# Kernel tuning notes

Hardware: AMD Instinct MI355X
Metric: run time of the kernel (lower is better)

## Reference

```python
import jax, jax.numpy as jnp
import numpy as np

N_NODES = 100000   # number of graph nodes
N_EDGES = 1600000  # adjacency nnz (avg degree 16)
FEAT_NNZ = 1600000 # sparse feature nnz (~16 per node)
F_IN = 512
F_OUT = 128


def setup_inputs() -> dict:
    key = jax.random.key(0)
    k1, k2, k3, k4, k5, k6 = jax.random.split(key, 6)
    adj_indices = jax.random.randint(k1, (2, N_EDGES), 0, N_NODES, dtype=jnp.int64 if jax.config.jax_enable_x64 else jnp.int32)
    adj_values = jax.random.uniform(k2, (N_EDGES,), dtype=jnp.float32)
    feat_rows = jax.random.randint(k3, (FEAT_NNZ,), 0, N_NODES)
    feat_cols = jax.random.randint(k4, (FEAT_NNZ,), 0, F_IN)
    feat_values = jax.random.uniform(k5, (FEAT_NNZ,), dtype=jnp.float32)
    # xavier_uniform init of the dense weight, as in the torch module
    bound = float(np.sqrt(6.0 / (F_IN + F_OUT)))
    weight = jax.random.uniform(k6, (F_IN, F_OUT), dtype=jnp.float32, minval=-bound, maxval=bound)
    return {
        "adj_indices": adj_indices,
        "adj_values": adj_values,
        "feat_rows": feat_rows,
        "feat_cols": feat_cols,
        "feat_values": feat_values,
        "weight": weight,
        "num_nodes": N_NODES,
    }


def _spmm(rows, cols, vals, num_rows, dense):
    """COO sparse [num_rows, ?] @ dense [?, K] -> [num_rows, K]."""
    msgs = vals[:, None] * dense[cols]          # [nnz, K] gather + scale
    return jax.ops.segment_sum(msgs, rows, num_segments=num_rows)


def reference(adj_indices, adj_values, feat_rows, feat_cols, feat_values, weight, num_nodes):
    # spmm(features, W): sparse [N, F_in] @ [F_in, F_out]
    base_features = _spmm(feat_rows, feat_cols, feat_values, num_nodes, weight)
    # spmm(A_hat, base): sparse [N, N] @ [N, F_out]  -- neighbor aggregation
    out = _spmm(adj_indices[0], adj_indices[1], adj_values, num_nodes, base_features)
    return out
```

## Files before the change

kernel.cpp:

```cpp
#include <hip/hip_runtime.h>
#include <stdint.h>

#define N_NODES 100000
#define F_IN    512
#define F_OUT   128
#define BROWS   128
#define NBKT    ((N_NODES + BROWS - 1) / BROWS)
#define CAP     2560
#define EPB     2048
#define WPAD    136

typedef unsigned short     u16;
typedef unsigned int       u32;
typedef unsigned long long u64;
typedef long long          i64;

__device__ __forceinline__ float b2f(u16 u) {
    union { u32 i; float f; } x; x.i = ((u32)u) << 16; return x.f;
}
__device__ __forceinline__ u16 f2b(float f) {
    u32 i = __float_as_uint(f);
    return (u16)((i + 0x7fffu + ((i >> 16) & 1u)) >> 16);
}
__device__ __forceinline__ float blo(u32 u) { return __uint_as_float(u << 16); }
__device__ __forceinline__ float bhi(u32 u) { return __uint_as_float(u & 0xFFFF0000u); }
__device__ __forceinline__ int ld_idx(const void* p, int i, int w64) {
    return w64 ? (int)((const i64*)p)[i] : ((const int*)p)[i];
}
__device__ __forceinline__ u16 ld_val_bf(const void* p, int i, int f32) {
    return f32 ? f2b(((const float*)p)[i]) : ((const u16*)p)[i];
}

__device__ __forceinline__ void ld_idx4(int* r, const void* p, int g, int w64) {
    if (w64) {
        const i64* q = (const i64*)p + 4 * (size_t)g;
        longlong2 a = *(const longlong2*)q;
        longlong2 b = *(const longlong2*)(q + 2);
        r[0] = (int)a.x; r[1] = (int)a.y; r[2] = (int)b.x; r[3] = (int)b.y;
    } else {
        int4 a = *(const int4*)((const int*)p + 4 * (size_t)g);
        r[0] = a.x; r[1] = a.y; r[2] = a.z; r[3] = a.w;
    }
}
__device__ __forceinline__ void ld_val4(u32* v, const void* p, int g, int f32) {
    if (f32) {
        float4 a = *(const float4*)((const float*)p + 4 * (size_t)g);
        v[0] = f2b(a.x); v[1] = f2b(a.y); v[2] = f2b(a.z); v[3] = f2b(a.w);
    } else {
        ushort4 a = *(const ushort4*)((const u16*)p + 4 * (size_t)g);
        v[0] = a.x; v[1] = a.y; v[2] = a.z; v[3] = a.w;
    }
}

__global__ void sniff_k(const u16* __restrict__ w, const u32* __restrict__ adj,
                        const u32* __restrict__ frows, int* __restrict__ flags,
                        int* __restrict__ gcurF, int* __restrict__ gcurA) {
    int t = threadIdx.x;
    if (t < 64) {
        u32 e0 = (w[t]      >> 7) & 0xFF;
        u32 e1 = (w[64 + t] >> 7) & 0xFF;
        u64 bad = __ballot((e0 > 0x7B) || (e1 > 0x7B));
        u64 za = __ballot(adj[2 * t + 1] == 0u);
        u64 zf = __ballot(frows[2 * t + 1] == 0u);
        if (t == 0) {
            flags[0] = (bad != 0);
            flags[1] = (__popcll(za) >= 32);
            flags[2] = (__popcll(zf) >= 32);
        }
    }
    for (int i = t; i < NBKT; i += 256) { gcurF[i] = 0; gcurA[i] = 0; }
}

__global__ __launch_bounds__(512, 4) void binFA_k(
        const void* __restrict__ frows, const void* __restrict__ fcols,
        const void* __restrict__ fvals, int M, int nFb,
        const void* __restrict__ adjbase, const void* __restrict__ avals, int E,
        const int* __restrict__ flags, int* __restrict__ gcurF, int* __restrict__ gcurA,
        u32* __restrict__ fbkt, u64* __restrict__ abkt) {
    __shared__ int hist[NBKT];
    __shared__ int hbase[NBKT];
    int t = threadIdx.x;
    for (int i = t; i < NBKT; i += 512) hist[i] = 0;
    __syncthreads();
    int f32 = flags[0];
    if ((int)blockIdx.x < nFb) {
        int f64 = flags[2];
        int start = blockIdx.x * EPB;
        int end = min(start + EPB, M);
        int g = (start >> 2) + t;
        int e0 = 4 * g;
        int r[4] = {-1, -1, -1, -1};
        int c[4]; u32 v[4];
        if (e0 + 3 < end) {
            ld_idx4(r, frows, g, f64);
            ld_idx4(c, fcols, g, f64);
            ld_val4(v, fvals, g, f32);
        } else {
            #pragma unroll
            for (int j = 0; j < 4; ++j) if (e0 + j < end) {
                r[j] = ld_idx(frows, e0 + j, f64);
                c[j] = ld_idx(fcols, e0 + j, f64);
                v[j] = ld_val_bf(fvals, e0 + j, f32);
            }
        }
        #pragma unroll
        for (int j = 0; j < 4; ++j) if (r[j] >= 0) atomicAdd(&hist[r[j] >> 7], 1);
        __syncthreads();
        for (int i = t; i < NBKT; i += 512) {
            int h = hist[i];
            hbase[i] = h ? atomicAdd(&gcurF[i], h) : 0;
            hist[i] = 0;
        }
        __syncthreads();
        #pragma unroll
        for (int j = 0; j < 4; ++j) if (r[j] >= 0) {
            int b = r[j] >> 7;
            int pos = hbase[b] + atomicAdd(&hist[b], 1);
            if (pos < CAP)
                fbkt[(size_t)b * CAP + pos] = (v[j] << 16) | ((u32)(r[j] & 127) << 9) | (u32)c[j];
        }
    } else {
        int a64 = flags[1];
        const void* acols = a64 ? (const void*)((const i64*)adjbase + E)
                                : (const void*)((const int*)adjbase + E);
        int start = ((int)blockIdx.x - nFb) * EPB;
        int end = min(start + EPB, E);
        int g = (start >> 2) + t;
        int e0 = 4 * g;
        int r[4] = {-1, -1, -1, -1};
        int c[4]; u32 v[4];
        if (e0 + 3 < end) {
            ld_idx4(r, adjbase, g, a64);
            ld_idx4(c, acols, g, a64);
            ld_val4(v, avals, g, f32);
        } else {
            #pragma unroll
            for (int j = 0; j < 4; ++j) if (e0 + j < end) {
                r[j] = ld_idx(adjbase, e0 + j, a64);
                c[j] = ld_idx(acols, e0 + j, a64);
                v[j] = ld_val_bf(avals, e0 + j, f32);
            }
        }
        #pragma unroll
        for (int j = 0; j < 4; ++j) if (r[j] >= 0) atomicAdd(&hist[r[j] >> 7], 1);
        __syncthreads();
        for (int i = t; i < NBKT; i += 512) {
            int h = hist[i];
            hbase[i] = h ? atomicAdd(&gcurA[i], h) : 0;
            hist[i] = 0;
        }
        __syncthreads();
        #pragma unroll
        for (int j = 0; j < 4; ++j) if (r[j] >= 0) {
            int b = r[j] >> 7;
            int pos = hbase[b] + atomicAdd(&hist[b], 1);
            if (pos < CAP)
                abkt[(size_t)b * CAP + pos] =
                    ((u64)v[j] << 24) | ((u64)(r[j] & 127) << 17) | (u64)(u32)c[j];
        }
    }
}

__global__ __launch_bounds__(512, 1) void stage1_k(const int* __restrict__ cnt,
        const u32* __restrict__ bkts, const void* __restrict__ W,
        const int* __restrict__ flags, u16* __restrict__ base) {
    __shared__ u16 Wlds[F_IN * WPAD];
    __shared__ u32 csr[CAP];
    __shared__ int hcnt[BROWS];
    __shared__ int roff[BROWS + 1];
    __shared__ int cur[BROWS];
    int t = threadIdx.x;
    int f32 = flags[0];
    if (!f32) {
        const u16* Wb = (const u16*)W;
        for (int idx = t; idx < F_IN * 16; idx += 512) {
            int r = idx >> 4, c = idx & 15;
            uint4 q = *(const uint4*)(Wb + r * F_OUT + c * 8);
            *(uint4*)&Wlds[r * WPAD + c * 8] = q;
        }
    }
    int w = t >> 6, lane = t & 63, g16 = lane >> 4, l16 = lane & 15;
    for (int b = blockIdx.x; b < NBKT; b += gridDim.x) {
        int n = cnt[b]; if (n > CAP) n = CAP;
        const u32* ed = bkts + (size_t)b * CAP;
        if (t < BROWS) hcnt[t] = 0;
        __syncthreads();
        u32 pb[5];
        #pragma unroll
        for (int k = 0; k < 5; ++k) { int i = t + k * 512; pb[k] = (i < n) ? ed[i] : 0u; }
        #pragma unroll
        for (int k = 0; k < 5; ++k) { int i = t + k * 512; if (i < n) atomicAdd(&hcnt[(pb[k] >> 9) & 127], 1); }
        __syncthreads();
        if (t < 64) {
            int h0 = hcnt[2 * t], h1 = hcnt[2 * t + 1];
            int s = h0 + h1, v2 = s;
            #pragma unroll
            for (int off = 1; off < 64; off <<= 1) {
                int u = __shfl_up(v2, off);
                if (t >= off) v2 += u;
            }
            int excl = v2 - s;
            roff[2 * t] = excl;     roff[2 * t + 1] = excl + h0;
            cur[2 * t]  = excl;     cur[2 * t + 1]  = excl + h0;
            if (t == 63) roff[128] = v2;
        }
        __syncthreads();
        #pragma unroll
        for (int k = 0; k < 5; ++k) {
            int i = t + k * 512;
            if (i < n) {
                u32 p = pb[k];
                int pos = atomicAdd(&cur[(p >> 9) & 127], 1);
                csr[pos] = p;
            }
        }
        __syncthreads();
        #pragma unroll
        for (int set = 0; set < 4; ++set) {
            int row = set * 32 + w * 4 + g16;
            int s = roff[row], e = roff[row + 1];
            float a0 = 0.f, a1 = 0.f, a2 = 0.f, a3 = 0.f, a4 = 0.f, a5 = 0.f, a6 = 0.f, a7 = 0.f;
            if (f32) {
                const float* Wf = (const float*)W;
                for (int j0 = s; j0 < e; j0 += 4) {
                    u32 p[4]; float4 qa[4], qb[4];
                    #pragma unroll
                    for (int k = 0; k < 4; ++k) { int jk = j0 + k; p[k] = csr[jk < e ? jk : e - 1]; }
                    #pragma unroll
                    for (int k = 0; k < 4; ++k) {
                        const float* wp = Wf + (size_t)(p[k] & 0x1FF) * F_OUT + l16 * 8;
                        qa[k] = *(const float4*)wp;
                        qb[k] = *(const float4*)(wp + 4);
                    }
                    #pragma unroll
                    for (int k = 0; k < 4; ++k) {
                        float v = (j0 + k < e) ? b2f((u16)(p[k] >> 16)) : 0.f;
                        a0 += v * qa[k].x; a1 += v * qa[k].y;
                        a2 += v * qa[k].z; a3 += v * qa[k].w;
                        a4 += v * qb[k].x; a5 += v * qb[k].y;
                        a6 += v * qb[k].z; a7 += v * qb[k].w;
                    }
                }
            } else {
                for (int j0 = s; j0 < e; j0 += 4) {
                    u32 p[4]; uint4 q[4];
                    #pragma unroll
                    for (int k = 0; k < 4; ++k) { int jk = j0 + k; p[k] = csr[jk < e ? jk : e - 1]; }
                    #pragma unroll
                    for (int k = 0; k < 4; ++k)
                        q[k] = *(const uint4*)&Wlds[(p[k] & 0x1FF) * WPAD + l16 * 8];
                    #pragma unroll
                    for (int k = 0; k < 4; ++k) {
                        float v = (j0 + k < e) ? b2f((u16)(p[k] >> 16)) : 0.f;
                        a0 += v * blo(q[k].x); a1 += v * bhi(q[k].x);
                        a2 += v * blo(q[k].y); a3 += v * bhi(q[k].y);
                        a4 += v * blo(q[k].z); a5 += v * bhi(q[k].z);
                        a6 += v * blo(q[k].w); a7 += v * bhi(q[k].w);
                    }
                }
            }
            int gr = b * BROWS + row;
            if (gr < N_NODES) {
                uint4 o;
                o.x = (u32)f2b(a0) | ((u32)f2b(a1) << 16);
                o.y = (u32)f2b(a2) | ((u32)f2b(a3) << 16);
                o.z = (u32)f2b(a4) | ((u32)f2b(a5) << 16);
                o.w = (u32)f2b(a6) | ((u32)f2b(a7) << 16);
                *(uint4*)(base + (size_t)gr * F_OUT + l16 * 8) = o;
            }
        }
        __syncthreads();
    }
}

__global__ __launch_bounds__(512, 4) void stage2_k(const int* __restrict__ cnt,
        const u64* __restrict__ bkts, const u16* __restrict__ base,
        const int* __restrict__ flags, void* __restrict__ out) {
    __shared__ u64 csr[CAP];
    __shared__ int hcnt[BROWS];
    __shared__ int roff[BROWS + 1];
    __shared__ int cur[BROWS];
    int t = threadIdx.x;
    int b = blockIdx.x;
    int n = cnt[b]; if (n > CAP) n = CAP;
    const u64* ed = bkts + (size_t)b * CAP;
    if (t < BROWS) hcnt[t] = 0;
    __syncthreads();
    u64 pb[5];
    #pragma unroll
    for (int k = 0; k < 5; ++k) { int i = t + k * 512; pb[k] = (i < n) ? ed[i] : 0ull; }
    #pragma unroll
    for (int k = 0; k < 5; ++k) { int i = t + k * 512; if (i < n) atomicAdd(&hcnt[(int)((pb[k] >> 17) & 127)], 1); }
    __syncthreads();
    if (t < 64) {
        int h0 = hcnt[2 * t], h1 = hcnt[2 * t + 1];
        int s = h0 + h1, v2 = s;
        #pragma unroll
        for (int off = 1; off < 64; off <<= 1) {
            int u = __shfl_up(v2, off);
            if (t >= off) v2 += u;
        }
        int excl = v2 - s;
        roff[2 * t] = excl;     roff[2 * t + 1] = excl + h0;
        cur[2 * t]  = excl;     cur[2 * t + 1]  = excl + h0;
        if (t == 63) roff[128] = v2;
    }
    __syncthreads();
    #pragma unroll
    for (int k = 0; k < 5; ++k) {
        int i = t + k * 512;
        if (i < n) {
            u64 p = pb[k];
            int pos = atomicAdd(&cur[(int)((p >> 17) & 127)], 1);
            csr[pos] = p;
        }
    }
    __syncthreads();
    int wave = t >> 6, lane = t & 63, g16 = lane >> 4, l16 = lane & 15;
    int f32o = flags[0];
    #pragma unroll
    for (int set = 0; set < 4; ++set) {
        int row = set * 32 + wave * 4 + g16;
        int s = roff[row], e = roff[row + 1];
        float a0 = 0.f, a1 = 0.f, a2 = 0.f, a3 = 0.f, a4 = 0.f, a5 = 0.f, a6 = 0.f, a7 = 0.f;
        for (int j0 = s; j0 < e; j0 += 8) {
            u64 p[8]; uint4 q[8];
            #pragma unroll
            for (int k = 0; k < 8; ++k) { int jk = j0 + k; p[k] = csr[jk < e ? jk : e - 1]; }
            #pragma unroll
            for (int k = 0; k < 8; ++k)
                q[k] = *(const uint4*)(base + (size_t)(u32)(p[k] & 0x1FFFF) * F_OUT + l16 * 8);
            #pragma unroll
            for (int k = 0; k < 8; ++k) {
                float v = (j0 + k < e) ? b2f((u16)(p[k] >> 24)) : 0.f;
                a0 += v * blo(q[k].x); a1 += v * bhi(q[k].x);
                a2 += v * blo(q[k].y); a3 += v * bhi(q[k].y);
                a4 += v * blo(q[k].z); a5 += v * bhi(q[k].z);
                a6 += v * blo(q[k].w); a7 += v * bhi(q[k].w);
            }
        }
        int gr = b * BROWS + row;
        if (gr < N_NODES) {
            if (f32o) {
                float* op = (float*)out + (size_t)gr * F_OUT + l16 * 8;
                float4 o0, o1;
                o0.x = a0; o0.y = a1; o0.z = a2; o0.w = a3;
                o1.x = a4; o1.y = a5; o1.z = a6; o1.w = a7;
                *(float4*)op = o0;
                *(float4*)(op + 4) = o1;
            } else {
                uint4 o;
                o.x = (u32)f2b(a0) | ((u32)f2b(a1) << 16);
                o.y = (u32)f2b(a2) | ((u32)f2b(a3) << 16);
                o.z = (u32)f2b(a4) | ((u32)f2b(a5) << 16);
                o.w = (u32)f2b(a6) | ((u32)f2b(a7) << 16);
                *(uint4*)((u16*)out + (size_t)gr * F_OUT + l16 * 8) = o;
            }
        }
    }
}

extern "C" void kernel_launch(void* const* d_in, const int* in_sizes, int n_in,
                              void* d_out, int out_size, void* d_ws, size_t ws_size,
                              hipStream_t stream) {
    const void* adj_idx   = d_in[0];
    const void* adj_vals  = d_in[1];
    const void* feat_rows = d_in[2];
    const void* feat_cols = d_in[3];
    const void* feat_vals = d_in[4];
    const void* weight    = d_in[5];

    const int E = in_sizes[0] / 2;
    const int M = in_sizes[2];

    char* ws = (char*)d_ws;
    size_t o = 0;
    auto alloc = [&](size_t b) { size_t r = o; o += (b + 255) & ~(size_t)255; return r; };
    int* gcurF = (int*)(ws + alloc((size_t)NBKT * 4));
    int* gcurA = (int*)(ws + alloc((size_t)NBKT * 4));
    int* flags = (int*)(ws + alloc(4 * 4));
    u32* fbkt  = (u32*)(ws + alloc((size_t)NBKT * CAP * 4));
    u64* abkt  = (u64*)(ws + alloc((size_t)NBKT * CAP * 8));
    u16* base  = (u16*)(ws + alloc((size_t)N_NODES * F_OUT * 2));
    (void)ws_size;

    const int nFb = (M + EPB - 1) / EPB;
    const int nAb = (E + EPB - 1) / EPB;

    sniff_k<<<1, 256, 0, stream>>>((const u16*)weight, (const u32*)adj_idx,
                                   (const u32*)feat_rows, flags, gcurF, gcurA);
    binFA_k<<<nFb + nAb, 512, 0, stream>>>(feat_rows, feat_cols, feat_vals, M, nFb,
                                           adj_idx, adj_vals, E,
                                           flags, gcurF, gcurA, fbkt, abkt);
    stage1_k<<<256, 512, 0, stream>>>(gcurF, fbkt, weight, flags, base);
    stage2_k<<<NBKT, 512, 0, stream>>>(gcurA, abkt, base, flags, d_out);
}
```

Measured before the change: 254.0 us.

## Fold dtype sniffing into kernels, memset counters, and double block sizes

Removes the separate sniff kernel: each kernel now recomputes the dtype/width flags itself into shared memory, and the bucket cursors are zeroed with hipMemsetAsync. The binning kernel moves to 1024-thread blocks, each handling 4096 edges, and stage1 moves to 1024 threads with fewer per-thread loop iterations. The aim is to cut a launch and inter-kernel dependency and to halve the binning grid, which also halves the global atomics on the bucket cursors. The cost is redundant sniff loads in every block and possibly lower occupancy from the larger blocks. In stage2, sf is written by wave 0 and read after existing barriers, so this appears safe.

```diff
diff --git a/kernel.cpp b/kernel.cpp
--- a/kernel.cpp
+++ b/kernel.cpp
@@ -7,7 +7,7 @@
 #define BROWS   128
 #define NBKT    ((N_NODES + BROWS - 1) / BROWS)
 #define CAP     2560
-#define EPB     2048
+#define EPB     4096
 #define WPAD    136
 
 typedef unsigned short     u16;
@@ -52,10 +52,8 @@
     }
 }
 
-__global__ void sniff_k(const u16* __restrict__ w, const u32* __restrict__ adj,
-                        const u32* __restrict__ frows, int* __restrict__ flags,
-                        int* __restrict__ gcurF, int* __restrict__ gcurA) {
-    int t = threadIdx.x;
+__device__ __forceinline__ void sniff3(const u16* w, const u32* adj, const u32* frows,
+                                       int* sf, int t) {
     if (t < 64) {
         u32 e0 = (w[t]      >> 7) & 0xFF;
         u32 e1 = (w[64 + t] >> 7) & 0xFF;
@@ -63,28 +61,30 @@
         u64 za = __ballot(adj[2 * t + 1] == 0u);
         u64 zf = __ballot(frows[2 * t + 1] == 0u);
         if (t == 0) {
-            flags[0] = (bad != 0);
-            flags[1] = (__popcll(za) >= 32);
-            flags[2] = (__popcll(zf) >= 32);
-        }
-    }
-    for (int i = t; i < NBKT; i += 256) { gcurF[i] = 0; gcurA[i] = 0; }
-}
-
-__global__ __launch_bounds__(512, 4) void binFA_k(
+            sf[0] = (bad != 0);
+            sf[1] = (__popcll(za) >= 32);
+            sf[2] = (__popcll(zf) >= 32);
+        }
+    }
+}
+
+__global__ __launch_bounds__(1024, 8) void binFA2_k(
         const void* __restrict__ frows, const void* __restrict__ fcols,
         const void* __restrict__ fvals, int M, int nFb,
         const void* __restrict__ adjbase, const void* __restrict__ avals, int E,
-        const int* __restrict__ flags, int* __restrict__ gcurF, int* __restrict__ gcurA,
+        const u16* __restrict__ weight,
+        int* __restrict__ gcurF, int* __restrict__ gcurA,
         u32* __restrict__ fbkt, u64* __restrict__ abkt) {
     __shared__ int hist[NBKT];
     __shared__ int hbase[NBKT];
+    __shared__ int sf[3];
     int t = threadIdx.x;
-    for (int i = t; i < NBKT; i += 512) hist[i] = 0;
-    __syncthreads();
-    int f32 = flags[0];
+    sniff3(weight, (const u32*)adjbase, (const u32*)frows, sf, t);
+    for (int i = t; i < NBKT; i += 1024) hist[i] = 0;
+    __syncthreads();
+    int f32 = sf[0];
     if ((int)blockIdx.x < nFb) {
-        int f64 = flags[2];
+        int f64 = sf[2];
         int start = blockIdx.x * EPB;
         int end = min(start + EPB, M);
         int g = (start >> 2) + t;
@@ -106,7 +106,7 @@
         #pragma unroll
         for (int j = 0; j < 4; ++j) if (r[j] >= 0) atomicAdd(&hist[r[j] >> 7], 1);
         __syncthreads();
-        for (int i = t; i < NBKT; i += 512) {
+        for (int i = t; i < NBKT; i += 1024) {
             int h = hist[i];
             hbase[i] = h ? atomicAdd(&gcurF[i], h) : 0;
             hist[i] = 0;
@@ -120,7 +120,7 @@
                 fbkt[(size_t)b * CAP + pos] = (v[j] << 16) | ((u32)(r[j] & 127) << 9) | (u32)c[j];
         }
     } else {
-        int a64 = flags[1];
+        int a64 = sf[1];
         const void* acols = a64 ? (const void*)((const i64*)adjbase + E)
                                 : (const void*)((const int*)adjbase + E);
         int start = ((int)blockIdx.x - nFb) * EPB;
@@ -144,7 +144,7 @@
         #pragma unroll
         for (int j = 0; j < 4; ++j) if (r[j] >= 0) atomicAdd(&hist[r[j] >> 7], 1);
         __syncthreads();
-        for (int i = t; i < NBKT; i += 512) {
+        for (int i = t; i < NBKT; i += 1024) {
             int h = hist[i];
             hbase[i] = h ? atomicAdd(&gcurA[i], h) : 0;
             hist[i] = 0;
@@ -161,19 +161,23 @@
     }
 }
 
-__global__ __launch_bounds__(512, 1) void stage1_k(const int* __restrict__ cnt,
+__global__ __launch_bounds__(1024, 1) void stage1_k(const int* __restrict__ cnt,
         const u32* __restrict__ bkts, const void* __restrict__ W,
-        const int* __restrict__ flags, u16* __restrict__ base) {
+        const u32* __restrict__ adjsn, const u32* __restrict__ frsn,
+        u16* __restrict__ base) {
     __shared__ u16 Wlds[F_IN * WPAD];
     __shared__ u32 csr[CAP];
     __shared__ int hcnt[BROWS];
     __shared__ int roff[BROWS + 1];
     __shared__ int cur[BROWS];
+    __shared__ int sf[3];
     int t = threadIdx.x;
-    int f32 = flags[0];
+    sniff3((const u16*)W, adjsn, frsn, sf, t);
+    __syncthreads();
+    int f32 = sf[0];
     if (!f32) {
         const u16* Wb = (const u16*)W;
-        for (int idx = t; idx < F_IN * 16; idx += 512) {
+        for (int idx = t; idx < F_IN * 16; idx += 1024) {
             int r = idx >> 4, c = idx & 15;
             uint4 q = *(const uint4*)(Wb + r * F_OUT + c * 8);
             *(uint4*)&Wlds[r * WPAD + c * 8] = q;
@@ -185,11 +189,11 @@
         const u32* ed = bkts + (size_t)b * CAP;
         if (t < BROWS) hcnt[t] = 0;
         __syncthreads();
-        u32 pb[5];
-        #pragma unroll
-        for (int k = 0; k < 5; ++k) { int i = t + k * 512; pb[k] = (i < n) ? ed[i] : 0u; }
-        #pragma unroll
-        for (int k = 0; k < 5; ++k) { int i = t + k * 512; if (i < n) atomicAdd(&hcnt[(pb[k] >> 9) & 127], 1); }
+        u32 pb[3];
+        #pragma unroll
+        for (int k = 0; k < 3; ++k) { int i = t + k * 1024; pb[k] = (i < n) ? ed[i] : 0u; }
+        #pragma unroll
+        for (int k = 0; k < 3; ++k) { int i = t + k * 1024; if (i < n) atomicAdd(&hcnt[(pb[k] >> 9) & 127], 1); }
         __syncthreads();
         if (t < 64) {
             int h0 = hcnt[2 * t], h1 = hcnt[2 * t + 1];
@@ -206,8 +210,8 @@
         }
         __syncthreads();
         #pragma unroll
-        for (int k = 0; k < 5; ++k) {
-            int i = t + k * 512;
+        for (int k = 0; k < 3; ++k) {
+            int i = t + k * 1024;
             if (i < n) {
                 u32 p = pb[k];
                 int pos = atomicAdd(&cur[(p >> 9) & 127], 1);
@@ -216,8 +220,8 @@
         }
         __syncthreads();
         #pragma unroll
-        for (int set = 0; set < 4; ++set) {
-            int row = set * 32 + w * 4 + g16;
+        for (int set = 0; set < 2; ++set) {
+            int row = set * 64 + w * 4 + g16;
             int s = roff[row], e = roff[row + 1];
             float a0 = 0.f, a1 = 0.f, a2 = 0.f, a3 = 0.f, a4 = 0.f, a5 = 0.f, a6 = 0.f, a7 = 0.f;
             if (f32) {
@@ -275,12 +279,15 @@
 
 __global__ __launch_bounds__(512, 4) void stage2_k(const int* __restrict__ cnt,
         const u64* __restrict__ bkts, const u16* __restrict__ base,
-        const int* __restrict__ flags, void* __restrict__ out) {
+        const void* __restrict__ W, const u32* __restrict__ adjsn,
+        const u32* __restrict__ frsn, void* __restrict__ out) {
     __shared__ u64 csr[CAP];
     __shared__ int hcnt[BROWS];
     __shared__ int roff[BROWS + 1];
     __shared__ int cur[BROWS];
+    __shared__ int sf[3];
     int t = threadIdx.x;
+    sniff3((const u16*)W, adjsn, frsn, sf, t);
     int b = blockIdx.x;
     int n = cnt[b]; if (n > CAP) n = CAP;
     const u64* ed = bkts + (size_t)b * CAP;
@@ -317,7 +324,7 @@
     }
     __syncthreads();
     int wave = t >> 6, lane = t & 63, g16 = lane >> 4, l16 = lane & 15;
-    int f32o = flags[0];
+    int f32o = sf[0];
     #pragma unroll
     for (int set = 0; set < 4; ++set) {
         int row = set * 32 + wave * 4 + g16;
@@ -378,7 +385,7 @@
     auto alloc = [&](size_t b) { size_t r = o; o += (b + 255) & ~(size_t)255; return r; };
     int* gcurF = (int*)(ws + alloc((size_t)NBKT * 4));
     int* gcurA = (int*)(ws + alloc((size_t)NBKT * 4));
-    int* flags = (int*)(ws + alloc(4 * 4));
+    size_t cur_end = o;
     u32* fbkt  = (u32*)(ws + alloc((size_t)NBKT * CAP * 4));
     u64* abkt  = (u64*)(ws + alloc((size_t)NBKT * CAP * 8));
     u16* base  = (u16*)(ws + alloc((size_t)N_NODES * F_OUT * 2));
@@ -387,11 +394,12 @@
     const int nFb = (M + EPB - 1) / EPB;
     const int nAb = (E + EPB - 1) / EPB;
 
-    sniff_k<<<1, 256, 0, stream>>>((const u16*)weight, (const u32*)adj_idx,
-                                   (const u32*)feat_rows, flags, gcurF, gcurA);
-    binFA_k<<<nFb + nAb, 512, 0, stream>>>(feat_rows, feat_cols, feat_vals, M, nFb,
-                                           adj_idx, adj_vals, E,
-                                           flags, gcurF, gcurA, fbkt, abkt);
-    stage1_k<<<256, 512, 0, stream>>>(gcurF, fbkt, weight, flags, base);
-    stage2_k<<<NBKT, 512, 0, stream>>>(gcurA, abkt, base, flags, d_out);
-}
+    hipMemsetAsync(ws, 0, cur_end, stream);
+    binFA2_k<<<nFb + nAb, 1024, 0, stream>>>(feat_rows, feat_cols, feat_vals, M, nFb,
+                                             adj_idx, adj_vals, E, (const u16*)weight,
+                                             gcurF, gcurA, fbkt, abkt);
+    stage1_k<<<256, 1024, 0, stream>>>(gcurF, fbkt, weight,
+                                       (const u32*)adj_idx, (const u32*)feat_rows, base);
+    stage2_k<<<NBKT, 512, 0, stream>>>(gcurA, abkt, base, weight,
+                                       (const u32*)adj_idx, (const u32*)feat_rows, d_out);
+}
```

Result: faster. 241.9 us (-4.7%).
